# Kernel optimization log

Measured on AMD Instinct MI355X. Metric: run time of the kernel, lower is better.

The kernel has to match this reference:

```python
import jax, jax.numpy as jnp
import numpy as np

B, S, D, H, DFF, L, R, V = 2, 1024, 1024, 16, 4096, 2, 3, 32000
HD = D // H


def layer_norm(x, g, b, eps=1e-5):
    mu = jnp.mean(x, axis=-1, keepdims=True)
    var = jnp.var(x, axis=-1, keepdims=True)
    return (x - mu) / jnp.sqrt(var + eps) * g + b


def recursion_block(x, mask, Wqkv, bqkv, Wo, bo, W1, b1, W2, b2, ln1_g, ln1_b, ln2_g, ln2_b):
    # shared pre-LN transformer stack of L layers, applied once per recursion step
    Bc, Sc, _ = x.shape
    scale = 1.0 / np.sqrt(HD).astype(np.float32)
    for l in range(L):
        h = layer_norm(x, ln1_g[l], ln1_b[l])
        qkv = h @ Wqkv[l] + bqkv[l]
        q, k, v = jnp.split(qkv, 3, axis=-1)
        q = q.reshape(Bc, Sc, H, HD).transpose(0, 2, 1, 3)
        k = k.reshape(Bc, Sc, H, HD).transpose(0, 2, 1, 3)
        v = v.reshape(Bc, Sc, H, HD).transpose(0, 2, 1, 3)
        scores = jnp.einsum('bhqd,bhkd->bhqk', q, k) * scale + mask
        attn = jax.nn.softmax(scores, axis=-1)
        o = jnp.einsum('bhqk,bhkd->bhqd', attn, v).transpose(0, 2, 1, 3).reshape(Bc, Sc, D)
        x = x + o @ Wo[l] + bo[l]
        h2 = layer_norm(x, ln2_g[l], ln2_b[l])
        x = x + jax.nn.gelu(h2 @ W1[l] + b1[l]) @ W2[l] + b2[l]
    return x


def setup_inputs() -> dict:
    key = jax.random.key(0)
    ks = jax.random.split(key, 12)
    n = lambda k, shape: (jax.random.normal(k, shape, jnp.float32) * 0.02)
    return {
        'input_ids': jax.random.randint(ks[0], (B, S), 0, V),
        'token_embed': n(ks[1], (V, D)),
        'pos_embed': n(ks[2], (S, D)),
        'Wqkv': n(ks[3], (L, D, 3 * D)), 'bqkv': jnp.zeros((L, 3 * D), jnp.float32),
        'Wo': n(ks[4], (L, D, D)), 'bo': jnp.zeros((L, D), jnp.float32),
        'W1': n(ks[5], (L, D, DFF)), 'b1': jnp.zeros((L, DFF), jnp.float32),
        'W2': n(ks[6], (L, DFF, D)), 'b2': jnp.zeros((L, D), jnp.float32),
        'ln1_g': jnp.ones((L, D), jnp.float32), 'ln1_b': jnp.zeros((L, D), jnp.float32),
        'ln2_g': jnp.ones((L, D), jnp.float32), 'ln2_b': jnp.zeros((L, D), jnp.float32),
        'final_g': jnp.ones((D,), jnp.float32), 'final_b': jnp.zeros((D,), jnp.float32),
        'Wr': n(ks[7], (D, R)), 'br': jnp.zeros((R,), jnp.float32),
    }


def reference(input_ids, token_embed, pos_embed, Wqkv, bqkv, Wo, bo, W1, b1, W2, b2,
              ln1_g, ln1_b, ln2_g, ln2_b, final_g, final_b, Wr, br):
    h = token_embed[input_ids] + pos_embed[None, :, :]            # [B,S,D]
    mask = jnp.where(jnp.tril(jnp.ones((S, S), bool)), 0.0, -jnp.inf)[None, None]  # [1,1,S,S]
    # token-choice router on detached hidden states
    rlogits = jax.lax.stop_gradient(h) @ Wr + br                  # [B,S,R]
    probs = jax.nn.softmax(rlogits, axis=-1)
    depth_map = jnp.argmax(rlogits, axis=-1) + 1                  # depths in 1..R
    importance = probs.mean(axis=(0, 1))
    router_loss = R * jnp.sum(importance ** 2)                    # load-balance aux loss
    res = h
    for step in range(R):
        step_mask = depth_map >= step + 1                         # [B,S] bool
        upd = recursion_block(res, mask, Wqkv, bqkv, Wo, bo, W1, b1, W2, b2,
                              ln1_g, ln1_b, ln2_g, ln2_b)
        res = jnp.where(step_mask[..., None], upd, res)
    hf = layer_norm(res, final_g, final_b)
    logits = hf @ token_embed.T                                   # tied lm_head
    return logits, depth_map, router_loss
```

## Files before the change

kernel.cpp:

```cpp
#include <hip/hip_runtime.h>
#include <hip/hip_bf16.h>

#define DD 1024
#define SS 1024
#define BB 2
#define HH 16
#define DFFN 4096
#define LLAYERS 2
#define RSTEPS 3
#define VV 32000
#define NTOK (BB*SS)

typedef __attribute__((ext_vector_type(8))) short s16x8;
typedef __attribute__((ext_vector_type(8))) __bf16 bf16x8;
typedef __attribute__((ext_vector_type(4))) float f32x4;

__device__ __forceinline__ unsigned short f2bf(float f) {
  unsigned int u = __float_as_uint(f);
  u += 0x7FFFu + ((u >> 16) & 1u);
  return (unsigned short)(u >> 16);
}

__device__ __forceinline__ f32x4 mfma16(s16x8 a, s16x8 b, f32x4 c) {
  return __builtin_amdgcn_mfma_f32_16x16x32_bf16(
      __builtin_bit_cast(bf16x8, a), __builtin_bit_cast(bf16x8, b), c, 0, 0, 0);
}

__device__ __forceinline__ void gload16(const unsigned short* g, unsigned short* l) {
  __builtin_amdgcn_global_load_lds(
      (const __attribute__((address_space(1))) unsigned int*)(const void*)g,
      (__attribute__((address_space(3))) unsigned int*)(void*)l, 16, 0, 0);
}

#define BAR()  asm volatile("s_barrier" ::: "memory")
#define LGK0() do { asm volatile("s_waitcnt lgkmcnt(0)" ::: "memory"); \
                    __builtin_amdgcn_sched_barrier(0); } while (0)
#define VM4()  asm volatile("s_waitcnt vmcnt(4)" ::: "memory")
#define VM0()  asm volatile("s_waitcnt vmcnt(0)" ::: "memory")

__global__ __launch_bounds__(256) void wtrans_all_kernel(
    const float* __restrict__ Wqkv, const float* __restrict__ Wo,
    const float* __restrict__ W1, const float* __restrict__ W2,
    unsigned short* __restrict__ WqkvT, unsigned short* __restrict__ WoT,
    unsigned short* __restrict__ W1T, unsigned short* __restrict__ W2T) {
  const int bid = blockIdx.x;
  const float* src; unsigned short* dst; int Kd, Nd, local;
  if (bid < 1536) {
    int l = bid >> 9 >= 1 ? (bid >= 768) : 0; l = (bid >= 768);
    local = bid - l * 768;
    src = Wqkv + (long)l * DD * 3 * DD; dst = WqkvT + (long)l * 3 * DD * DD;
    Kd = DD; Nd = 3 * DD;
  } else if (bid < 2048) {
    int l = (bid - 1536) >> 8; local = (bid - 1536) & 255;
    src = Wo + (long)l * DD * DD; dst = WoT + (long)l * DD * DD;
    Kd = DD; Nd = DD;
  } else if (bid < 4096) {
    int l = (bid - 2048) >> 10; local = (bid - 2048) & 1023;
    src = W1 + (long)l * DD * DFFN; dst = W1T + (long)l * DFFN * DD;
    Kd = DD; Nd = DFFN;
  } else {
    int l = (bid - 4096) >> 10; local = (bid - 4096) & 1023;
    src = W2 + (long)l * DFFN * DD; dst = W2T + (long)l * DD * DFFN;
    Kd = DFFN; Nd = DD;
  }
  const int tn = Nd >> 6;
  const int n0 = (local % tn) * 64, k0 = (local / tn) * 64;
  __shared__ unsigned short t[64][68];
  const int tid = threadIdx.x;
#pragma unroll
  for (int c = 0; c < 4; ++c) {
    int p = tid + c * 256;
    int kr = p >> 4, nc = (p & 15) * 4;
    float4 v = *(const float4*)(src + (long)(k0 + kr) * Nd + n0 + nc);
    t[nc + 0][kr] = f2bf(v.x);
    t[nc + 1][kr] = f2bf(v.y);
    t[nc + 2][kr] = f2bf(v.z);
    t[nc + 3][kr] = f2bf(v.w);
  }
  __syncthreads();
#pragma unroll
  for (int c = 0; c < 4; ++c) {
    int p = tid + c * 256;
    int nr = p >> 4, kc = (p & 15) * 4;
    ushort4 o;
    o.x = t[nr][kc]; o.y = t[nr][kc + 1]; o.z = t[nr][kc + 2]; o.w = t[nr][kc + 3];
    *(ushort4*)(dst + (long)(n0 + nr) * Kd + k0 + kc) = o;
  }
}

__global__ __launch_bounds__(256) void bconv_kernel(
    const float* __restrict__ src, unsigned short* __restrict__ dst) {
  long i = ((long)blockIdx.x * 256 + threadIdx.x) * 8;
  float4 v0 = *(const float4*)(src + i);
  float4 v1 = *(const float4*)(src + i + 4);
  ushort4 a, b;
  a.x = f2bf(v0.x); a.y = f2bf(v0.y); a.z = f2bf(v0.z); a.w = f2bf(v0.w);
  b.x = f2bf(v1.x); b.y = f2bf(v1.y); b.z = f2bf(v1.z); b.w = f2bf(v1.w);
  *(ushort4*)(dst + i) = a;
  *(ushort4*)(dst + i + 4) = b;
}

__global__ __launch_bounds__(256) void embed_router_kernel(
    const int* __restrict__ ids, const float* __restrict__ te,
    const float* __restrict__ pe, const float* __restrict__ Wr,
    const float* __restrict__ br, float* __restrict__ res,
    float* __restrict__ probs, float* __restrict__ depth_ws,
    float* __restrict__ out_depth) {
  int row = blockIdx.x;
  int s = row & (SS - 1);
  int id = ids[row];
  int t = threadIdx.x;
  int d = t * 4;
  float4 a = *(const float4*)(te + (long)id * DD + d);
  float4 p = *(const float4*)(pe + (long)s * DD + d);
  float4 o; o.x = a.x + p.x; o.y = a.y + p.y; o.z = a.z + p.z; o.w = a.w + p.w;
  *(float4*)(res + (long)row * DD + d) = o;
  float a0 = 0.f, a1 = 0.f, a2 = 0.f;
  float hv[4] = {o.x, o.y, o.z, o.w};
#pragma unroll
  for (int j = 0; j < 4; ++j) {
    int dd = d + j;
    a0 += hv[j] * Wr[dd * 3 + 0];
    a1 += hv[j] * Wr[dd * 3 + 1];
    a2 += hv[j] * Wr[dd * 3 + 2];
  }
  for (int off = 32; off; off >>= 1) {
    a0 += __shfl_down(a0, off);
    a1 += __shfl_down(a1, off);
    a2 += __shfl_down(a2, off);
  }
  __shared__ float red[4][3];
  int wave = t >> 6;
  if ((t & 63) == 0) { red[wave][0] = a0; red[wave][1] = a1; red[wave][2] = a2; }
  __syncthreads();
  if (t == 0) {
    a0 = red[0][0] + red[1][0] + red[2][0] + red[3][0] + br[0];
    a1 = red[0][1] + red[1][1] + red[2][1] + red[3][1] + br[1];
    a2 = red[0][2] + red[1][2] + red[2][2] + red[3][2] + br[2];
    float m = fmaxf(a0, fmaxf(a1, a2));
    float e0 = expf(a0 - m), e1 = expf(a1 - m), e2 = expf(a2 - m);
    float inv = 1.f / (e0 + e1 + e2);
    probs[row * 3 + 0] = e0 * inv;
    probs[row * 3 + 1] = e1 * inv;
    probs[row * 3 + 2] = e2 * inv;
    int am = 0; float bv = a0;
    if (a1 > bv) { bv = a1; am = 1; }
    if (a2 > bv) { bv = a2; am = 2; }
    float dm = (float)(am + 1);
    depth_ws[row] = dm;
    out_depth[row] = dm;
  }
}

__global__ __launch_bounds__(256) void router_finalize_kernel(
    const float* __restrict__ probs, float* __restrict__ out_loss) {
  __shared__ float red[256][3];
  int t = threadIdx.x;
  float s0 = 0.f, s1 = 0.f, s2 = 0.f;
  for (int r = t; r < NTOK; r += 256) {
    s0 += probs[r * 3 + 0]; s1 += probs[r * 3 + 1]; s2 += probs[r * 3 + 2];
  }
  red[t][0] = s0; red[t][1] = s1; red[t][2] = s2;
  __syncthreads();
  for (int off = 128; off; off >>= 1) {
    if (t < off) {
      red[t][0] += red[t + off][0];
      red[t][1] += red[t + off][1];
      red[t][2] += red[t + off][2];
    }
    __syncthreads();
  }
  if (t == 0) {
    float i0 = red[0][0] / NTOK, i1 = red[0][1] / NTOK, i2 = red[0][2] / NTOK;
    out_loss[0] = (float)RSTEPS * (i0 * i0 + i1 * i1 + i2 * i2);
  }
}

__global__ __launch_bounds__(256) void ln_kernel(
    const float* __restrict__ x, const float* __restrict__ g,
    const float* __restrict__ b, unsigned short* __restrict__ y) {
  int row = blockIdx.x;
  int t = threadIdx.x;
  float4 v = *(const float4*)(x + (long)row * DD + t * 4);
  float s = v.x + v.y + v.z + v.w;
  float q = v.x * v.x + v.y * v.y + v.z * v.z + v.w * v.w;
  for (int off = 32; off; off >>= 1) {
    s += __shfl_down(s, off);
    q += __shfl_down(q, off);
  }
  __shared__ float rs[4], rq[4];
  int wave = t >> 6;
  if ((t & 63) == 0) { rs[wave] = s; rq[wave] = q; }
  __syncthreads();
  float S_ = rs[0] + rs[1] + rs[2] + rs[3];
  float Q_ = rq[0] + rq[1] + rq[2] + rq[3];
  float mu = S_ * (1.f / DD);
  float var = Q_ * (1.f / DD) - mu * mu;
  float rstd = rsqrtf(var + 1e-5f);
  int d = t * 4;
  float4 gg = *(const float4*)(g + d);
  float4 bb = *(const float4*)(b + d);
  ushort4 ov;
  ov.x = f2bf((v.x - mu) * rstd * gg.x + bb.x);
  ov.y = f2bf((v.y - mu) * rstd * gg.y + bb.y);
  ov.z = f2bf((v.z - mu) * rstd * gg.z + bb.z);
  ov.w = f2bf((v.w - mu) * rstd * gg.w + bb.w);
  *(ushort4*)(y + (long)row * DD + d) = ov;
}

__device__ __forceinline__ void stageA8(unsigned short* S, int buf, int qm,
    const unsigned short* A, int lda, long m0, int kt, int tid) {
  unsigned short* dst = S + buf * 32768 + qm * 8192;
#pragma unroll
  for (int c = 0; c < 2; ++c) {
    int idx = tid + c * 512;
    int L = (idx << 4) ^ (((idx >> 5) & 1) << 5);
    int band = L >> 13, row = (L >> 7) & 63, kel = (L & 127) >> 1;
    gload16(A + (m0 + band * 128 + qm * 64 + row) * (long)lda + kt * 64 + kel,
            dst + idx * 8);
  }
}

__device__ __forceinline__ void stageB8(unsigned short* S, int buf, int qn,
    const unsigned short* Bt, int ldb, long n0, int kt, int tid) {
  unsigned short* dst = S + buf * 32768 + 16384 + qn * 8192;
#pragma unroll
  for (int c = 0; c < 2; ++c) {
    int idx = tid + c * 512;
    int L = (idx << 4) ^ (((idx >> 5) & 1) << 5);
    int band = L >> 12, row = (L >> 7) & 31, kel = (L & 127) >> 1;
    gload16(Bt + (n0 + band * 64 + qn * 32 + row) * (long)ldb + kt * 64 + kel,
            dst + idx * 8);
  }
}

__device__ __forceinline__ void read_af8(const unsigned short* S, int base,
    int wm, int l16, int g, s16x8 af[2][4]) {
  const int swz = ((l16 >> 2) & 1) << 5;
#pragma unroll
  for (int kk = 0; kk < 2; ++kk)
#pragma unroll
    for (int mf = 0; mf < 4; ++mf) {
      int L = (wm * 8192 + (mf * 16 + l16) * 128 + (kk * 32 + g * 8) * 2) ^ swz;
      af[kk][mf] = *(const s16x8*)(S + base + (L >> 1));
    }
}

__device__ __forceinline__ void read_bf8(const unsigned short* S, int base,
    int wn, int l16, int g, s16x8 bf[2][2]) {
  const int swz = ((l16 >> 2) & 1) << 5;
#pragma unroll
  for (int kk = 0; kk < 2; ++kk)
#pragma unroll
    for (int nf = 0; nf < 2; ++nf) {
      int L = (wn * 4096 + (nf * 16 + l16) * 128 + (kk * 32 + g * 8) * 2) ^ swz;
      bf[kk][nf] = *(const s16x8*)(S + base + (L >> 1));
    }
}

template<int QM, int QN>
__device__ __forceinline__ void do_mfma8(f32x4 acc[8][4],
    const s16x8 af[2][4], const s16x8 bf[2][2]) {
  __builtin_amdgcn_s_setprio(1);
#pragma unroll
  for (int kk = 0; kk < 2; ++kk)
#pragma unroll
    for (int mf = 0; mf < 4; ++mf)
#pragma unroll
      for (int nf = 0; nf < 2; ++nf)
        acc[QM * 4 + mf][QN * 2 + nf] =
            mfma16(af[kk][mf], bf[kk][nf], acc[QM * 4 + mf][QN * 2 + nf]);
  __builtin_amdgcn_s_setprio(0);
}

template<int CBF16, int BIAS, int GELU_ACT>
__global__ __launch_bounds__(512, 1) void gemm256_kernel(
    const unsigned short* __restrict__ A, int lda,
    const unsigned short* __restrict__ Bt, int ldb,
    void* __restrict__ Cv, int ldc,
    const float* __restrict__ bias, int K, int Mblocks) {
  __shared__ unsigned short S[65536];
  const int tid = threadIdx.x;
  const int lane = tid & 63, wave = tid >> 6;
  const int g = lane >> 4, l16 = lane & 15;
  const int wm = wave >> 2, wn = wave & 3;
  const int nwg = gridDim.x * gridDim.y;
  const int orig = blockIdx.x + blockIdx.y * gridDim.x;
  const int q = nwg >> 3, r = nwg & 7;
  const int xcd = orig & 7, loc = orig >> 3;
  const int wgid = (xcd < r ? xcd * (q + 1) : r * (q + 1) + (xcd - r) * q) + loc;
  const long m0 = (long)(wgid % Mblocks) * 256;
  const long n0 = (long)(wgid / Mblocks) * 256;

  f32x4 acc[8][4] = {};
  s16x8 af[2][4], bf[2][2];
  const int NI = K >> 7;

  stageA8(S, 0, 0, A, lda, m0, 0, tid);
  stageA8(S, 0, 1, A, lda, m0, 0, tid);
  stageB8(S, 0, 0, Bt, ldb, n0, 0, tid);
  stageB8(S, 0, 1, Bt, ldb, n0, 0, tid);
  stageA8(S, 1, 0, A, lda, m0, 1, tid);
  stageB8(S, 1, 1, Bt, ldb, n0, 1, tid);
  VM4(); BAR();

  for (int i = 0; i < NI; ++i) {
    const int kt1 = 2 * i + 1, kt2 = 2 * i + 2, kt3 = 2 * i + 3;
    const bool more = (i + 1 < NI);
    read_af8(S, 0, wm, l16, g, af);
    read_bf8(S, 16384, wn, l16, g, bf);
    stageA8(S, 1, 1, A, lda, m0, kt1, tid);
    BAR(); LGK0();
    do_mfma8<0, 0>(acc, af, bf);
    BAR();
    read_bf8(S, 16384 + 8192, wn, l16, g, bf);
    stageB8(S, 1, 0, Bt, ldb, n0, kt1, tid);
    BAR(); LGK0();
    do_mfma8<0, 1>(acc, af, bf);
    BAR();
    read_af8(S, 8192, wm, l16, g, af);
    if (more) stageA8(S, 0, 0, A, lda, m0, kt2, tid);
    BAR(); LGK0();
    do_mfma8<1, 1>(acc, af, bf);
    BAR();
    read_bf8(S, 16384, wn, l16, g, bf);
    if (more) stageB8(S, 0, 1, Bt, ldb, n0, kt2, tid);
    BAR(); LGK0();
    do_mfma8<1, 0>(acc, af, bf);
    if (more) { VM4(); } else { VM0(); }
    BAR();
    read_af8(S, 32768, wm, l16, g, af);
    read_bf8(S, 32768 + 16384, wn, l16, g, bf);
    if (more) stageA8(S, 0, 1, A, lda, m0, kt2, tid);
    BAR(); LGK0();
    do_mfma8<0, 0>(acc, af, bf);
    BAR();
    read_bf8(S, 32768 + 16384 + 8192, wn, l16, g, bf);
    if (more) stageB8(S, 0, 0, Bt, ldb, n0, kt2, tid);
    BAR(); LGK0();
    do_mfma8<0, 1>(acc, af, bf);
    BAR();
    read_af8(S, 32768 + 8192, wm, l16, g, af);
    if (more) stageA8(S, 1, 0, A, lda, m0, kt3, tid);
    BAR(); LGK0();
    do_mfma8<1, 1>(acc, af, bf);
    BAR();
    read_bf8(S, 32768 + 16384, wn, l16, g, bf);
    if (more) stageB8(S, 1, 1, Bt, ldb, n0, kt3, tid);
    BAR(); LGK0();
    do_mfma8<1, 0>(acc, af, bf);
    VM4(); BAR();
  }

#pragma unroll
  for (int mf = 0; mf < 8; ++mf) {
#pragma unroll
    for (int nf = 0; nf < 4; ++nf) {
      long row0 = m0 + wm * 128 + mf * 16 + g * 4;
      long col = n0 + wn * 64 + nf * 16 + l16;
      float bv = BIAS ? bias[col] : 0.f;
#pragma unroll
      for (int rr = 0; rr < 4; ++rr) {
        float v = acc[mf][nf][rr] + bv;
        if (GELU_ACT) {
          float x3 = v * v * v;
          v = 0.5f * v * (1.f + tanhf(0.7978845608028654f * (v + 0.044715f * x3)));
        }
        if (CBF16) ((unsigned short*)Cv)[(row0 + rr) * (long)ldc + col] = f2bf(v);
        else       ((float*)Cv)[(row0 + rr) * (long)ldc + col] = v;
      }
    }
  }
}

template<int BN, int CBF16, int BIAS, int RESID, int GELU_ACT, int SELW>
__global__ __launch_bounds__(256) void gemm128_kernel(
    const unsigned short* __restrict__ A, int lda,
    const unsigned short* __restrict__ Bt, int ldb,
    void* __restrict__ Cv, int ldc,
    const float* __restrict__ bias,
    const float* __restrict__ resid, int ldr,
    const float* __restrict__ depth_ws, float stepf,
    int K) {
  constexpr int BM = 128;
  constexpr int WN = BN / 2;
  constexpr int MR = 4;
  constexpr int NR = WN / 16;
  __shared__ unsigned short As[BM * 64];
  __shared__ unsigned short Bs[BN * 64];
  const int tid = threadIdx.x;
  const int lane = tid & 63, wave = tid >> 6;
  const int g = lane >> 4, l16 = lane & 15;
  const int wr = wave >> 1, wc = wave & 1;
  int lin = blockIdx.x + blockIdx.y * gridDim.x;
  int per = (gridDim.x * gridDim.y) >> 3;
  int v = (lin & 7) * per + (lin >> 3);
  const long m0 = (long)(v % gridDim.y) * BM;
  const long n0 = (long)(v / gridDim.y) * BN;
  f32x4 acc[MR][NR] = {};
  for (int k0 = 0; k0 < K; k0 += 64) {
    __syncthreads();
#pragma unroll
    for (int c = 0; c < BM / 32; ++c) {
      int p = tid + c * 256;
      int r = p >> 3, kq = (p & 7) * 8;
      gload16(A + (m0 + r) * (long)lda + k0 + kq, &As[p * 8]);
    }
#pragma unroll
    for (int c = 0; c < BN / 32; ++c) {
      int p = tid + c * 256;
      int r = p >> 3, kq = (p & 7) * 8;
      gload16(Bt + (n0 + r) * (long)ldb + k0 + kq, &Bs[p * 8]);
    }
    __syncthreads();
#pragma unroll
    for (int kk = 0; kk < 2; ++kk) {
      s16x8 af[MR], bf[NR];
#pragma unroll
      for (int m = 0; m < MR; ++m)
        af[m] = *(const s16x8*)&As[(wr * 64 + m * 16 + l16) * 64 + kk * 32 + g * 8];
#pragma unroll
      for (int n = 0; n < NR; ++n)
        bf[n] = *(const s16x8*)&Bs[(wc * WN + n * 16 + l16) * 64 + kk * 32 + g * 8];
#pragma unroll
      for (int m = 0; m < MR; ++m)
#pragma unroll
        for (int n = 0; n < NR; ++n)
          acc[m][n] = mfma16(af[m], bf[n], acc[m][n]);
    }
  }
#pragma unroll
  for (int m = 0; m < MR; ++m) {
#pragma unroll
    for (int n = 0; n < NR; ++n) {
      long row_base = m0 + wr * 64 + m * 16 + g * 4;
      long col = n0 + wc * WN + n * 16 + l16;
      float bv = BIAS ? bias[col] : 0.f;
#pragma unroll
      for (int r = 0; r < 4; ++r) {
        long row = row_base + r;
        float vv = acc[m][n][r] + bv;
        if (RESID) vv += resid[row * (long)ldr + col];
        if (GELU_ACT) {
          float x3 = vv * vv * vv;
          vv = 0.5f * vv * (1.f + tanhf(0.7978845608028654f * (vv + 0.044715f * x3)));
        }
        if (SELW) {
          if (depth_ws[row] >= stepf)
            ((float*)Cv)[row * (long)ldc + col] = vv;
        } else if (CBF16) {
          ((unsigned short*)Cv)[row * (long)ldc + col] = f2bf(vv);
        } else {
          ((float*)Cv)[row * (long)ldc + col] = vv;
        }
      }
    }
  }
}

__global__ __launch_bounds__(256) void vtrans_kernel(
    const unsigned short* __restrict__ qkv, unsigned short* __restrict__ vt) {
  __shared__ unsigned short t[64][72];
  const int s0 = blockIdx.x * 64;
  const int bh = blockIdx.y;
  const int b = bh >> 4, h = bh & 15;
  const int tid = threadIdx.x;
  const long rowbase = (long)b * SS;
#pragma unroll
  for (int c = 0; c < 2; ++c) {
    int p = tid + c * 256;
    int sr = p >> 3, d8 = (p & 7) * 8;
    s16x8 v = *(const s16x8*)(qkv + (rowbase + s0 + sr) * 3072 + 2048 + h * 64 + d8);
#pragma unroll
    for (int j = 0; j < 8; ++j) t[d8 + j][sr] = v[j];
  }
  __syncthreads();
#pragma unroll
  for (int c = 0; c < 2; ++c) {
    int p = tid + c * 256;
    int d = p >> 3, s8 = (p & 7) * 8;
    *(s16x8*)(vt + ((long)bh * 64 + d) * SS + s0 + s8) = *(const s16x8*)&t[d][s8];
  }
}

__global__ __launch_bounds__(256) void attn_kernel(
    const unsigned short* __restrict__ qkv,
    const unsigned short* __restrict__ vt,
    unsigned short* __restrict__ o) {
  __shared__ unsigned short Ks[2][64 * 64];
  __shared__ unsigned short Vs[2][64 * 64];
  __shared__ unsigned short Pl[4][16][72];
  const int qb = blockIdx.x;
  const int bh = blockIdx.y;
  const int b = bh >> 4, h = bh & 15;
  const int tid = threadIdx.x, wave = tid >> 6, lane = tid & 63;
  const int g = lane >> 4, l16 = lane & 15;
  const float NEG_INF = -__builtin_inff();
  const int q0 = qb * 64;
  const int qrw = q0 + wave * 16;
  const long rowbase = (long)b * SS;
  const unsigned short* kbase = qkv + rowbase * 3072 + 1024 + h * 64;
  const unsigned short* vbase = vt + (long)bh * 64 * SS;

  const unsigned short* qptr = qkv + (rowbase + qrw + l16) * 3072 + h * 64;
  s16x8 qf0 = *(const s16x8*)(qptr + g * 8);
  s16x8 qf1 = *(const s16x8*)(qptr + 32 + g * 8);

  f32x4 oacc[4] = {};
  float mrun = NEG_INF, lrun = 0.f;

  const int ntile = q0 / 64 + 1;

#pragma unroll
  for (int c = 0; c < 2; ++c) {
    int idx = tid + c * 256;
    int r = idx >> 3;
    int bo = (idx & 7) * 16;
    int sw = (bo ^ ((r & 7) << 4)) >> 1;
    gload16(kbase + (long)r * 3072 + sw, &Ks[0][idx * 8]);
    gload16(vbase + (long)r * SS + 0 + sw, &Vs[0][idx * 8]);
  }
  asm volatile("s_waitcnt vmcnt(0)" ::: "memory");
  __syncthreads();

  for (int t = 0; t < ntile; ++t) {
    const int cur = t & 1;
    const int kv0 = t * 64;
    const unsigned short* ks_cur = &Ks[cur][0];
    const unsigned short* vs_cur = &Vs[cur][0];
    if (t + 1 < ntile) {
      const int kvn = kv0 + 64;
#pragma unroll
      for (int c = 0; c < 2; ++c) {
        int idx = tid + c * 256;
        int r = idx >> 3;
        int bo = (idx & 7) * 16;
        int sw = (bo ^ ((r & 7) << 4)) >> 1;
        gload16(kbase + (long)(kvn + r) * 3072 + sw, &Ks[cur ^ 1][idx * 8]);
        gload16(vbase + (long)r * SS + kvn + sw, &Vs[cur ^ 1][idx * 8]);
      }
    }
    f32x4 accs[4] = {};
#pragma unroll
    for (int ks = 0; ks < 2; ++ks) {
#pragma unroll
      for (int kvb = 0; kvb < 4; ++kvb) {
        int row = kvb * 16 + l16;
        int bo = ((ks * 64 + g * 16) ^ ((l16 & 7) << 4)) >> 1;
        s16x8 kf = *(const s16x8*)&ks_cur[row * 64 + bo];
        accs[kvb] = mfma16(kf, ks ? qf1 : qf0, accs[kvb]);
      }
    }
    const bool needmask = (kv0 + 63 > qrw);
    const int qabs = qrw + l16;
    float sv[4][4];
    float mloc = NEG_INF;
#pragma unroll
    for (int kvb = 0; kvb < 4; ++kvb) {
#pragma unroll
      for (int r = 0; r < 4; ++r) {
        float vv = accs[kvb][r] * 0.125f;
        if (needmask) {
          int kva = kv0 + kvb * 16 + g * 4 + r;
          if (kva > qabs) vv = NEG_INF;
        }
        sv[kvb][r] = vv;
        mloc = fmaxf(mloc, vv);
      }
    }
    mloc = fmaxf(mloc, __shfl_xor(mloc, 16));
    mloc = fmaxf(mloc, __shfl_xor(mloc, 32));
    float mnew = fmaxf(mrun, mloc);
    float alpha = __expf(mrun - mnew);
    float lsum = 0.f;
#pragma unroll
    for (int kvb = 0; kvb < 4; ++kvb) {
      float p0 = __expf(sv[kvb][0] - mnew);
      float p1 = __expf(sv[kvb][1] - mnew);
      float p2 = __expf(sv[kvb][2] - mnew);
      float p3 = __expf(sv[kvb][3] - mnew);
      lsum += (p0 + p1) + (p2 + p3);
      unsigned int w0 = (unsigned)f2bf(p0) | ((unsigned)f2bf(p1) << 16);
      unsigned int w1 = (unsigned)f2bf(p2) | ((unsigned)f2bf(p3) << 16);
      uint2 pw; pw.x = w0; pw.y = w1;
      *(uint2*)&Pl[wave][l16][kvb * 16 + g * 4] = pw;
    }
    lsum += __shfl_xor(lsum, 16);
    lsum += __shfl_xor(lsum, 32);
    lrun = lrun * alpha + lsum;
    mrun = mnew;
    float mult[4];
#pragma unroll
    for (int r = 0; r < 4; ++r) mult[r] = __shfl(alpha, g * 4 + r);
#pragma unroll
    for (int nd = 0; nd < 4; ++nd)
#pragma unroll
      for (int r = 0; r < 4; ++r) oacc[nd][r] *= mult[r];
#pragma unroll
    for (int kh = 0; kh < 2; ++kh) {
      s16x8 pa = *(const s16x8*)&Pl[wave][l16][kh * 32 + g * 8];
#pragma unroll
      for (int nd = 0; nd < 4; ++nd) {
        int row = nd * 16 + l16;
        int bo = ((kh * 64 + g * 16) ^ ((l16 & 7) << 4)) >> 1;
        s16x8 vf = *(const s16x8*)&vs_cur[row * 64 + bo];
        oacc[nd] = mfma16(pa, vf, oacc[nd]);
      }
    }
    asm volatile("s_waitcnt vmcnt(0)" ::: "memory");
    __syncthreads();
  }
  unsigned short* ob = o + (rowbase + qrw) * 1024 + h * 64;
#pragma unroll
  for (int r = 0; r < 4; ++r) {
    float lr = __shfl(lrun, g * 4 + r);
    float inv = 1.f / lr;
#pragma unroll
    for (int nd = 0; nd < 4; ++nd)
      ob[(long)(g * 4 + r) * 1024 + nd * 16 + l16] = f2bf(oacc[nd][r] * inv);
  }
}

extern "C" void kernel_launch(void* const* d_in, const int* in_sizes, int n_in,
                              void* d_out, int out_size, void* d_ws, size_t ws_size,
                              hipStream_t stream) {
  (void)in_sizes; (void)n_in; (void)out_size; (void)ws_size;
  const int*   ids  = (const int*)d_in[0];
  const float* te   = (const float*)d_in[1];
  const float* pe   = (const float*)d_in[2];
  const float* Wqkv = (const float*)d_in[3];
  const float* bqkv = (const float*)d_in[4];
  const float* Wo   = (const float*)d_in[5];
  const float* bo   = (const float*)d_in[6];
  const float* W1   = (const float*)d_in[7];
  const float* b1   = (const float*)d_in[8];
  const float* W2   = (const float*)d_in[9];
  const float* b2   = (const float*)d_in[10];
  const float* ln1g = (const float*)d_in[11];
  const float* ln1b = (const float*)d_in[12];
  const float* ln2g = (const float*)d_in[13];
  const float* ln2b = (const float*)d_in[14];
  const float* fing = (const float*)d_in[15];
  const float* finb = (const float*)d_in[16];
  const float* Wr   = (const float*)d_in[17];
  const float* br   = (const float*)d_in[18];

  float* logits    = (float*)d_out;
  float* out_depth = logits + (long)NTOK * VV;
  float* out_loss  = out_depth + NTOK;

  char* w = (char*)d_ws;
  float* res            = (float*)w;          w += (long)NTOK * DD * 4;
  float* x              = (float*)w;          w += (long)NTOK * DD * 4;
  unsigned short* hbuf  = (unsigned short*)w; w += (long)NTOK * DD * 2;
  unsigned short* qkvb  = (unsigned short*)w; w += (long)NTOK * 3 * DD * 2;
  unsigned short* obuf  = (unsigned short*)w; w += (long)NTOK * DD * 2;
  unsigned short* ffn1  = (unsigned short*)w; w += (long)NTOK * DFFN * 2;
  unsigned short* vtb   = (unsigned short*)w; w += (long)BB * HH * 64 * SS * 2;
  float* probs          = (float*)w;          w += (long)NTOK * 3 * 4;
  float* depth_ws       = (float*)w;          w += (long)NTOK * 4;
  unsigned short* WqkvT = (unsigned short*)w; w += (long)LLAYERS * 3 * DD * DD * 2;
  unsigned short* WoT   = (unsigned short*)w; w += (long)LLAYERS * DD * DD * 2;
  unsigned short* W1T   = (unsigned short*)w; w += (long)LLAYERS * DFFN * DD * 2;
  unsigned short* W2T   = (unsigned short*)w; w += (long)LLAYERS * DD * DFFN * 2;
  unsigned short* teb   = (unsigned short*)w; w += (long)VV * DD * 2;

  wtrans_all_kernel<<<6144, 256, 0, stream>>>(Wqkv, Wo, W1, W2,
                                              WqkvT, WoT, W1T, W2T);
  bconv_kernel<<<(long)VV * DD / 2048, 256, 0, stream>>>(te, teb);

  embed_router_kernel<<<NTOK, 256, 0, stream>>>(ids, te, pe, Wr, br,
                                                res, probs, depth_ws, out_depth);
  router_finalize_kernel<<<1, 256, 0, stream>>>(probs, out_loss);

  for (int step = 0; step < RSTEPS; ++step) {
    for (int l = 0; l < LLAYERS; ++l) {
      const float* xin = (l == 0) ? res : x;
      ln_kernel<<<NTOK, 256, 0, stream>>>(xin, ln1g + l * DD, ln1b + l * DD, hbuf);
      gemm128_kernel<128, 1, 1, 0, 0, 0><<<dim3(3 * DD / 128, NTOK / 128), 256, 0, stream>>>(
          hbuf, DD, WqkvT + (long)l * 3 * DD * DD, DD, qkvb, 3 * DD,
          bqkv + (long)l * 3 * DD, nullptr, 0, nullptr, 0.f, DD);
      vtrans_kernel<<<dim3(SS / 64, BB * HH), 256, 0, stream>>>(qkvb, vtb);
      attn_kernel<<<dim3(SS / 64, BB * HH), 256, 0, stream>>>(qkvb, vtb, obuf);
      gemm128_kernel<64, 0, 1, 1, 0, 0><<<dim3(DD / 64, NTOK / 128), 256, 0, stream>>>(
          obuf, DD, WoT + (long)l * DD * DD, DD, x, DD,
          bo + (long)l * DD, xin, DD, nullptr, 0.f, DD);
      ln_kernel<<<NTOK, 256, 0, stream>>>(x, ln2g + l * DD, ln2b + l * DD, hbuf);
      gemm128_kernel<128, 1, 1, 0, 1, 0><<<dim3(DFFN / 128, NTOK / 128), 256, 0, stream>>>(
          hbuf, DD, W1T + (long)l * DFFN * DD, DD, ffn1, DFFN,
          b1 + (long)l * DFFN, nullptr, 0, nullptr, 0.f, DD);
      if (l == 0) {
        gemm128_kernel<64, 0, 1, 1, 0, 0><<<dim3(DD / 64, NTOK / 128), 256, 0, stream>>>(
            ffn1, DFFN, W2T + (long)l * DD * DFFN, DFFN, x, DD,
            b2 + (long)l * DD, x, DD, nullptr, 0.f, DFFN);
      } else {
        gemm128_kernel<64, 0, 1, 1, 0, 1><<<dim3(DD / 64, NTOK / 128), 256, 0, stream>>>(
            ffn1, DFFN, W2T + (long)l * DD * DFFN, DFFN, res, DD,
            b2 + (long)l * DD, x, DD, depth_ws, (float)(step + 1), DFFN);
      }
    }
  }
  ln_kernel<<<NTOK, 256, 0, stream>>>(res, fing, finb, hbuf);
  gemm256_kernel<0, 0, 0><<<dim3(VV / 256, NTOK / 256), 512, 0, stream>>>(
      hbuf, DD, teb, DD, logits, VV, nullptr, DD, NTOK / 256);
}
```

Measured before the change: 1.460 ms.

## Fuse prep kernels, write V transposed from QKV GEMM, add 8-wave N=1024 GEMM

Merges weight transpose, embedding bf16 conversion and embed/router into one prep launch. The QKV GEMM epilogue now writes the V part straight into the transposed per-head layout, so the separate vtrans kernel goes away. The N=1024 projections (Wo, W2) move to a new 512-thread 8-wave GEMM with XCD-aware block swizzling. The attention grid is reversed so the longest causal blocks start first. These cut launch count and extra memory passes, in exchange for scattered 8-byte V stores and a new GEMM whose loads are not double-buffered.

```diff
diff --git a/kernel.cpp b/kernel.cpp
--- a/kernel.cpp
+++ b/kernel.cpp
@@ -38,15 +38,80 @@
 #define VM4()  asm volatile("s_waitcnt vmcnt(4)" ::: "memory")
 #define VM0()  asm volatile("s_waitcnt vmcnt(0)" ::: "memory")
 
-__global__ __launch_bounds__(256) void wtrans_all_kernel(
+__global__ __launch_bounds__(256) void prep_all_kernel(
     const float* __restrict__ Wqkv, const float* __restrict__ Wo,
     const float* __restrict__ W1, const float* __restrict__ W2,
+    const float* __restrict__ te,
     unsigned short* __restrict__ WqkvT, unsigned short* __restrict__ WoT,
-    unsigned short* __restrict__ W1T, unsigned short* __restrict__ W2T) {
+    unsigned short* __restrict__ W1T, unsigned short* __restrict__ W2T,
+    unsigned short* __restrict__ teb,
+    const int* __restrict__ ids, const float* __restrict__ pe,
+    const float* __restrict__ Wr, const float* __restrict__ br,
+    float* __restrict__ res, float* __restrict__ probs,
+    float* __restrict__ depth_ws, float* __restrict__ out_depth) {
   const int bid = blockIdx.x;
+  const int tid = threadIdx.x;
+  __shared__ unsigned short t[64][68];
+  __shared__ float red[4][3];
+  if (bid >= 22144) {
+    int row = bid - 22144;
+    int s = row & (SS - 1);
+    int id = ids[row];
+    int d = tid * 4;
+    float4 a = *(const float4*)(te + (long)id * DD + d);
+    float4 p = *(const float4*)(pe + (long)s * DD + d);
+    float4 o; o.x = a.x + p.x; o.y = a.y + p.y; o.z = a.z + p.z; o.w = a.w + p.w;
+    *(float4*)(res + (long)row * DD + d) = o;
+    float a0 = 0.f, a1 = 0.f, a2 = 0.f;
+    float hv[4] = {o.x, o.y, o.z, o.w};
+#pragma unroll
+    for (int j = 0; j < 4; ++j) {
+      int dd = d + j;
+      a0 += hv[j] * Wr[dd * 3 + 0];
+      a1 += hv[j] * Wr[dd * 3 + 1];
+      a2 += hv[j] * Wr[dd * 3 + 2];
+    }
+    for (int off = 32; off; off >>= 1) {
+      a0 += __shfl_down(a0, off);
+      a1 += __shfl_down(a1, off);
+      a2 += __shfl_down(a2, off);
+    }
+    int wave = tid >> 6;
+    if ((tid & 63) == 0) { red[wave][0] = a0; red[wave][1] = a1; red[wave][2] = a2; }
+    __syncthreads();
+    if (tid == 0) {
+      a0 = red[0][0] + red[1][0] + red[2][0] + red[3][0] + br[0];
+      a1 = red[0][1] + red[1][1] + red[2][1] + red[3][1] + br[1];
+      a2 = red[0][2] + red[1][2] + red[2][2] + red[3][2] + br[2];
+      float m = fmaxf(a0, fmaxf(a1, a2));
+      float e0 = expf(a0 - m), e1 = expf(a1 - m), e2 = expf(a2 - m);
+      float inv = 1.f / (e0 + e1 + e2);
+      probs[row * 3 + 0] = e0 * inv;
+      probs[row * 3 + 1] = e1 * inv;
+      probs[row * 3 + 2] = e2 * inv;
+      int am = 0; float bv = a0;
+      if (a1 > bv) { bv = a1; am = 1; }
+      if (a2 > bv) { bv = a2; am = 2; }
+      float dm = (float)(am + 1);
+      depth_ws[row] = dm;
+      out_depth[row] = dm;
+    }
+    return;
+  }
+  if (bid >= 6144) {
+    long i = ((long)(bid - 6144) * 256 + tid) * 8;
+    float4 v0 = *(const float4*)(te + i);
+    float4 v1 = *(const float4*)(te + i + 4);
+    ushort4 a, b;
+    a.x = f2bf(v0.x); a.y = f2bf(v0.y); a.z = f2bf(v0.z); a.w = f2bf(v0.w);
+    b.x = f2bf(v1.x); b.y = f2bf(v1.y); b.z = f2bf(v1.z); b.w = f2bf(v1.w);
+    *(ushort4*)(teb + i) = a;
+    *(ushort4*)(teb + i + 4) = b;
+    return;
+  }
   const float* src; unsigned short* dst; int Kd, Nd, local;
   if (bid < 1536) {
-    int l = bid >> 9 >= 1 ? (bid >= 768) : 0; l = (bid >= 768);
+    int l = (bid >= 768);
     local = bid - l * 768;
     src = Wqkv + (long)l * DD * 3 * DD; dst = WqkvT + (long)l * 3 * DD * DD;
     Kd = DD; Nd = 3 * DD;
@@ -65,8 +130,6 @@
   }
   const int tn = Nd >> 6;
   const int n0 = (local % tn) * 64, k0 = (local / tn) * 64;
-  __shared__ unsigned short t[64][68];
-  const int tid = threadIdx.x;
 #pragma unroll
   for (int c = 0; c < 4; ++c) {
     int p = tid + c * 256;
@@ -85,70 +148,6 @@
     ushort4 o;
     o.x = t[nr][kc]; o.y = t[nr][kc + 1]; o.z = t[nr][kc + 2]; o.w = t[nr][kc + 3];
     *(ushort4*)(dst + (long)(n0 + nr) * Kd + k0 + kc) = o;
-  }
-}
-
-__global__ __launch_bounds__(256) void bconv_kernel(
-    const float* __restrict__ src, unsigned short* __restrict__ dst) {
-  long i = ((long)blockIdx.x * 256 + threadIdx.x) * 8;
-  float4 v0 = *(const float4*)(src + i);
-  float4 v1 = *(const float4*)(src + i + 4);
-  ushort4 a, b;
-  a.x = f2bf(v0.x); a.y = f2bf(v0.y); a.z = f2bf(v0.z); a.w = f2bf(v0.w);
-  b.x = f2bf(v1.x); b.y = f2bf(v1.y); b.z = f2bf(v1.z); b.w = f2bf(v1.w);
-  *(ushort4*)(dst + i) = a;
-  *(ushort4*)(dst + i + 4) = b;
-}
-
-__global__ __launch_bounds__(256) void embed_router_kernel(
-    const int* __restrict__ ids, const float* __restrict__ te,
-    const float* __restrict__ pe, const float* __restrict__ Wr,
-    const float* __restrict__ br, float* __restrict__ res,
-    float* __restrict__ probs, float* __restrict__ depth_ws,
-    float* __restrict__ out_depth) {
-  int row = blockIdx.x;
-  int s = row & (SS - 1);
-  int id = ids[row];
-  int t = threadIdx.x;
-  int d = t * 4;
-  float4 a = *(const float4*)(te + (long)id * DD + d);
-  float4 p = *(const float4*)(pe + (long)s * DD + d);
-  float4 o; o.x = a.x + p.x; o.y = a.y + p.y; o.z = a.z + p.z; o.w = a.w + p.w;
-  *(float4*)(res + (long)row * DD + d) = o;
-  float a0 = 0.f, a1 = 0.f, a2 = 0.f;
-  float hv[4] = {o.x, o.y, o.z, o.w};
-#pragma unroll
-  for (int j = 0; j < 4; ++j) {
-    int dd = d + j;
-    a0 += hv[j] * Wr[dd * 3 + 0];
-    a1 += hv[j] * Wr[dd * 3 + 1];
-    a2 += hv[j] * Wr[dd * 3 + 2];
-  }
-  for (int off = 32; off; off >>= 1) {
-    a0 += __shfl_down(a0, off);
-    a1 += __shfl_down(a1, off);
-    a2 += __shfl_down(a2, off);
-  }
-  __shared__ float red[4][3];
-  int wave = t >> 6;
-  if ((t & 63) == 0) { red[wave][0] = a0; red[wave][1] = a1; red[wave][2] = a2; }
-  __syncthreads();
-  if (t == 0) {
-    a0 = red[0][0] + red[1][0] + red[2][0] + red[3][0] + br[0];
-    a1 = red[0][1] + red[1][1] + red[2][1] + red[3][1] + br[1];
-    a2 = red[0][2] + red[1][2] + red[2][2] + red[3][2] + br[2];
-    float m = fmaxf(a0, fmaxf(a1, a2));
-    float e0 = expf(a0 - m), e1 = expf(a1 - m), e2 = expf(a2 - m);
-    float inv = 1.f / (e0 + e1 + e2);
-    probs[row * 3 + 0] = e0 * inv;
-    probs[row * 3 + 1] = e1 * inv;
-    probs[row * 3 + 2] = e2 * inv;
-    int am = 0; float bv = a0;
-    if (a1 > bv) { bv = a1; am = 1; }
-    if (a2 > bv) { bv = a2; am = 2; }
-    float dm = (float)(am + 1);
-    depth_ws[row] = dm;
-    out_depth[row] = dm;
   }
 }
 
@@ -373,14 +372,14 @@
   }
 }
 
-template<int BN, int CBF16, int BIAS, int RESID, int GELU_ACT, int SELW>
+template<int BN, int CBF16, int BIAS, int RESID, int GELU_ACT, int QKVW>
 __global__ __launch_bounds__(256) void gemm128_kernel(
     const unsigned short* __restrict__ A, int lda,
     const unsigned short* __restrict__ Bt, int ldb,
     void* __restrict__ Cv, int ldc,
     const float* __restrict__ bias,
     const float* __restrict__ resid, int ldr,
-    const float* __restrict__ depth_ws, float stepf,
+    unsigned short* __restrict__ vtw,
     int K) {
   constexpr int BM = 128;
   constexpr int WN = BN / 2;
@@ -429,6 +428,7 @@
           acc[m][n] = mfma16(af[m], bf[n], acc[m][n]);
     }
   }
+  const bool vblk = QKVW && (n0 >= 2048);
 #pragma unroll
   for (int m = 0; m < MR; ++m) {
 #pragma unroll
@@ -436,6 +436,7 @@
       long row_base = m0 + wr * 64 + m * 16 + g * 4;
       long col = n0 + wc * WN + n * 16 + l16;
       float bv = BIAS ? bias[col] : 0.f;
+      float vv4[4];
 #pragma unroll
       for (int r = 0; r < 4; ++r) {
         long row = row_base + r;
@@ -445,6 +446,91 @@
           float x3 = vv * vv * vv;
           vv = 0.5f * vv * (1.f + tanhf(0.7978845608028654f * (vv + 0.044715f * x3)));
         }
+        vv4[r] = vv;
+      }
+      if (QKVW && vblk) {
+        int rel = (int)col - 2048;
+        int h = rel >> 6, d = rel & 63;
+        int b = (int)(row_base >> 10);
+        int s = (int)(row_base & 1023);
+        ushort4 o;
+        o.x = f2bf(vv4[0]); o.y = f2bf(vv4[1]);
+        o.z = f2bf(vv4[2]); o.w = f2bf(vv4[3]);
+        *(ushort4*)(vtw + (((long)(b * 16 + h) * 64 + d) * SS + s)) = o;
+      } else {
+#pragma unroll
+        for (int r = 0; r < 4; ++r) {
+          long row = row_base + r;
+          if (CBF16) ((unsigned short*)Cv)[row * (long)ldc + col] = f2bf(vv4[r]);
+          else       ((float*)Cv)[row * (long)ldc + col] = vv4[r];
+        }
+      }
+    }
+  }
+}
+
+template<int CBF16, int BIAS, int RESID, int SELW>
+__global__ __launch_bounds__(512) void gemm64w8_kernel(
+    const unsigned short* __restrict__ A, int lda,
+    const unsigned short* __restrict__ Bt, int ldb,
+    void* __restrict__ Cv, int ldc,
+    const float* __restrict__ bias,
+    const float* __restrict__ resid, int ldr,
+    const float* __restrict__ depth_ws, float stepf,
+    int K) {
+  __shared__ unsigned short As[128 * 64];
+  __shared__ unsigned short Bs[64 * 64];
+  const int tid = threadIdx.x;
+  const int lane = tid & 63, wave = tid >> 6;
+  const int g = lane >> 4, l16 = lane & 15;
+  const int wr = wave >> 1, wc = wave & 1;
+  int lin = blockIdx.x + blockIdx.y * gridDim.x;
+  int per = (gridDim.x * gridDim.y) >> 3;
+  int v = (lin & 7) * per + (lin >> 3);
+  const long m0 = (long)(v % gridDim.y) * 128;
+  const long n0 = (long)(v / gridDim.y) * 64;
+  f32x4 acc[2][2] = {};
+  for (int k0 = 0; k0 < K; k0 += 64) {
+    __syncthreads();
+#pragma unroll
+    for (int c = 0; c < 2; ++c) {
+      int p = tid + c * 512;
+      int r = p >> 3, kq = (p & 7) * 8;
+      gload16(A + (m0 + r) * (long)lda + k0 + kq, &As[p * 8]);
+    }
+    {
+      int r = tid >> 3, kq = (tid & 7) * 8;
+      gload16(Bt + (n0 + r) * (long)ldb + k0 + kq, &Bs[tid * 8]);
+    }
+    __syncthreads();
+#pragma unroll
+    for (int kk = 0; kk < 2; ++kk) {
+      s16x8 af[2], bf[2];
+#pragma unroll
+      for (int m = 0; m < 2; ++m)
+        af[m] = *(const s16x8*)&As[(wr * 32 + m * 16 + l16) * 64 + kk * 32 + g * 8];
+#pragma unroll
+      for (int n = 0; n < 2; ++n)
+        bf[n] = *(const s16x8*)&Bs[(wc * 32 + n * 16 + l16) * 64 + kk * 32 + g * 8];
+#pragma unroll
+      for (int m = 0; m < 2; ++m)
+#pragma unroll
+        for (int n = 0; n < 2; ++n)
+          acc[m][n] = mfma16(af[m], bf[n], acc[m][n]);
+    }
+  }
+#pragma unroll
+  for (int m = 0; m < 2; ++m) {
+#pragma unroll
+    for (int n = 0; n < 2; ++n) {
+      long row_base = m0 + wr * 32 + m * 16 + g * 4;
+      long col = n0 + wc * 32 + n * 16 + l16;
+      float bv = BIAS ? bias[col] : 0.f;
+#pragma unroll
+      for (int r = 0; r < 4; ++r) {
+        long row = row_base + r;
+        float vv = acc[m][n][r] + bv;
+        if (RESID) vv += resid[row * (long)ldr + col];
         if (SELW) {
           if (depth_ws[row] >= stepf)
             ((float*)Cv)[row * (long)ldc + col] = vv;
@@ -458,31 +544,6 @@
   }
 }
 
-__global__ __launch_bounds__(256) void vtrans_kernel(
-    const unsigned short* __restrict__ qkv, unsigned short* __restrict__ vt) {
-  __shared__ unsigned short t[64][72];
-  const int s0 = blockIdx.x * 64;
-  const int bh = blockIdx.y;
-  const int b = bh >> 4, h = bh & 15;
-  const int tid = threadIdx.x;
-  const long rowbase = (long)b * SS;
-#pragma unroll
-  for (int c = 0; c < 2; ++c) {
-    int p = tid + c * 256;
-    int sr = p >> 3, d8 = (p & 7) * 8;
-    s16x8 v = *(const s16x8*)(qkv + (rowbase + s0 + sr) * 3072 + 2048 + h * 64 + d8);
-#pragma unroll
-    for (int j = 0; j < 8; ++j) t[d8 + j][sr] = v[j];
-  }
-  __syncthreads();
-#pragma unroll
-  for (int c = 0; c < 2; ++c) {
-    int p = tid + c * 256;
-    int d = p >> 3, s8 = (p & 7) * 8;
-    *(s16x8*)(vt + ((long)bh * 64 + d) * SS + s0 + s8) = *(const s16x8*)&t[d][s8];
-  }
-}
-
 __global__ __launch_bounds__(256) void attn_kernel(
     const unsigned short* __restrict__ qkv,
     const unsigned short* __restrict__ vt,
@@ -490,7 +551,7 @@
   __shared__ unsigned short Ks[2][64 * 64];
   __shared__ unsigned short Vs[2][64 * 64];
   __shared__ unsigned short Pl[4][16][72];
-  const int qb = blockIdx.x;
+  const int qb = gridDim.x - 1 - blockIdx.x;
   const int bh = blockIdx.y;
   const int b = bh >> 4, h = bh & 15;
   const int tid = threadIdx.x, wave = tid >> 6, lane = tid & 63;
@@ -665,36 +726,32 @@
   unsigned short* W2T   = (unsigned short*)w; w += (long)LLAYERS * DD * DFFN * 2;
   unsigned short* teb   = (unsigned short*)w; w += (long)VV * DD * 2;
 
-  wtrans_all_kernel<<<6144, 256, 0, stream>>>(Wqkv, Wo, W1, W2,
-                                              WqkvT, WoT, W1T, W2T);
-  bconv_kernel<<<(long)VV * DD / 2048, 256, 0, stream>>>(te, teb);
-
-  embed_router_kernel<<<NTOK, 256, 0, stream>>>(ids, te, pe, Wr, br,
-                                                res, probs, depth_ws, out_depth);
+  prep_all_kernel<<<6144 + 16000 + NTOK, 256, 0, stream>>>(
+      Wqkv, Wo, W1, W2, te, WqkvT, WoT, W1T, W2T, teb,
+      ids, pe, Wr, br, res, probs, depth_ws, out_depth);
   router_finalize_kernel<<<1, 256, 0, stream>>>(probs, out_loss);
 
   for (int step = 0; step < RSTEPS; ++step) {
     for (int l = 0; l < LLAYERS; ++l) {
       const float* xin = (l == 0) ? res : x;
       ln_kernel<<<NTOK, 256, 0, stream>>>(xin, ln1g + l * DD, ln1b + l * DD, hbuf);
-      gemm128_kernel<128, 1, 1, 0, 0, 0><<<dim3(3 * DD / 128, NTOK / 128), 256, 0, stream>>>(
+      gemm128_kernel<128, 1, 1, 0, 0, 1><<<dim3(3 * DD / 128, NTOK / 128), 256, 0, stream>>>(
           hbuf, DD, WqkvT + (long)l * 3 * DD * DD, DD, qkvb, 3 * DD,
-          bqkv + (long)l * 3 * DD, nullptr, 0, nullptr, 0.f, DD);
-      vtrans_kernel<<<dim3(SS / 64, BB * HH), 256, 0, stream>>>(qkvb, vtb);
+          bqkv + (long)l * 3 * DD, nullptr, 0, vtb, DD);
       attn_kernel<<<dim3(SS / 64, BB * HH), 256, 0, stream>>>(qkvb, vtb, obuf);
-      gemm128_kernel<64, 0, 1, 1, 0, 0><<<dim3(DD / 64, NTOK / 128), 256, 0, stream>>>(
+      gemm64w8_kernel<0, 1, 1, 0><<<dim3(DD / 64, NTOK / 128), 512, 0, stream>>>(
           obuf, DD, WoT + (long)l * DD * DD, DD, x, DD,
           bo + (long)l * DD, xin, DD, nullptr, 0.f, DD);
       ln_kernel<<<NTOK, 256, 0, stream>>>(x, ln2g + l * DD, ln2b + l * DD, hbuf);
       gemm128_kernel<128, 1, 1, 0, 1, 0><<<dim3(DFFN / 128, NTOK / 128), 256, 0, stream>>>(
           hbuf, DD, W1T + (long)l * DFFN * DD, DD, ffn1, DFFN,
-          b1 + (long)l * DFFN, nullptr, 0, nullptr, 0.f, DD);
+          b1 + (long)l * DFFN, nullptr, 0, nullptr, DD);
       if (l == 0) {
-        gemm128_kernel<64, 0, 1, 1, 0, 0><<<dim3(DD / 64, NTOK / 128), 256, 0, stream>>>(
+        gemm64w8_kernel<0, 1, 1, 0><<<dim3(DD / 64, NTOK / 128), 512, 0, stream>>>(
             ffn1, DFFN, W2T + (long)l * DD * DFFN, DFFN, x, DD,
             b2 + (long)l * DD, x, DD, nullptr, 0.f, DFFN);
       } else {
-        gemm128_kernel<64, 0, 1, 1, 0, 1><<<dim3(DD / 64, NTOK / 128), 256, 0, stream>>>(
+        gemm64w8_kernel<0, 1, 1, 1><<<dim3(DD / 64, NTOK / 128), 512, 0, stream>>>(
             ffn1, DFFN, W2T + (long)l * DD * DFFN, DFFN, res, DD,
             b2 + (long)l * DD, x, DD, depth_ws, (float)(step + 1), DFFN);
       }
```

Measured after the change: 1.464 ms. About the same (+0.3%).
